# Kernel tuning notes

Hardware: AMD Instinct MI355X
Metric: run time of the kernel (lower is better)

The kernel has to match this reference:

```python
import jax, jax.numpy as jnp
import numpy as np

EMB = 64       # embedding_size
ATT = 32       # att_embedding_size (per-head dim)
HEADS = 4      # head_num
OUT = ATT * HEADS


def setup_inputs() -> dict:
    key = jax.random.key(0)
    ks = jax.random.split(key, 9)
    B, F = 16384, 40
    x = jax.random.normal(ks[0], (B, F, EMB), dtype=jnp.float32)
    # nn.Linear params: weight [out, in], bias [out]
    s = 0.05
    Wq = jax.random.normal(ks[1], (OUT, EMB), dtype=jnp.float32) * s
    bq = jax.random.normal(ks[2], (OUT,), dtype=jnp.float32) * s
    Wk = jax.random.normal(ks[3], (OUT, EMB), dtype=jnp.float32) * s
    bk = jax.random.normal(ks[4], (OUT,), dtype=jnp.float32) * s
    Wv = jax.random.normal(ks[5], (OUT, EMB), dtype=jnp.float32) * s
    bv = jax.random.normal(ks[6], (OUT,), dtype=jnp.float32) * s
    Wr = jax.random.normal(ks[7], (OUT, EMB), dtype=jnp.float32) * s
    br = jax.random.normal(ks[8], (OUT,), dtype=jnp.float32) * s
    return {"x": x, "Wq": Wq, "bq": bq, "Wk": Wk, "bk": bk,
            "Wv": Wv, "bv": bv, "Wr": Wr, "br": br}


def reference(x, Wq, bq, Wk, bk, Wv, bv, Wr, br):
    B, F, E = x.shape
    H, D = HEADS, ATT
    # QKV projections; split along last dim + cat along batch == reshape to heads
    q = (jnp.einsum('bfe,oe->bfo', x, Wq) + bq).reshape(B, F, H, D)
    k = (jnp.einsum('bfe,oe->bfo', x, Wk) + bk).reshape(B, F, H, D)
    v = (jnp.einsum('bfe,oe->bfo', x, Wv) + bv).reshape(B, F, H, D)
    # scaled dot-product attention over fields; NOTE: original scales by
    # sqrt(embedding_size), not sqrt(att_embedding_size)
    scale = 1.0 / jnp.sqrt(jnp.float32(E))
    att = jnp.einsum('bfhd,bghd->bhfg', q, k) * scale  # [B,H,F,F]
    att = jax.nn.softmax(att, axis=-1)                 # dropout_p = 0.0
    out = jnp.einsum('bhfg,bghd->bfhd', att, v).reshape(B, F, H * D)
    res = jnp.einsum('bfe,oe->bfo', x, Wr) + br        # use_res=True
    return jax.nn.relu(out + res)
```

## Files before the change

### kernel.cpp

```cpp
#include <hip/hip_runtime.h>
#include <hip/hip_bf16.h>


#define F_DIM 40
#define O_DIM 128

typedef __bf16 bf16x8 __attribute__((ext_vector_type(8)));
typedef __bf16 bf16x2 __attribute__((ext_vector_type(2)));
typedef float  f32x4  __attribute__((ext_vector_type(4)));

#define XBS 68
#define QS  40
#define VTS 72
#define OSS 44
#define HB0 3264
#define HSZ 5504
#define TOT 25280

static __device__ __forceinline__ unsigned pk2(float a, float b) {
  bf16x2 t;
  t[0] = (__bf16)a;
  t[1] = (__bf16)b;
  return __builtin_bit_cast(unsigned, t);
}
union V8 { uint2 u2[2]; uint4 u4; unsigned u[4]; bf16x8 v; };
static __device__ __forceinline__ bf16x8 lds_ld8(const unsigned short* p) {
  V8 t; t.u2[0] = *(const uint2*)p; t.u2[1] = *(const uint2*)(p + 4); return t.v;
}
static __device__ __forceinline__ bf16x8 lds_ld16(const unsigned short* p) {
  V8 t; t.u4 = *(const uint4*)p; return t.v;
}
static __device__ __forceinline__ f32x4 mfma16(bf16x8 a, bf16x8 b, f32x4 c) {
  return __builtin_amdgcn_mfma_f32_16x16x32_bf16(a, b, c, 0, 0, 0);
}

#if __has_builtin(__builtin_amdgcn_exp2f)
#define EXP2F __builtin_amdgcn_exp2f
#else
#define EXP2F exp2f
#endif
#if __has_builtin(__builtin_amdgcn_rcpf)
#define RCPF __builtin_amdgcn_rcpf
#else
#define RCPF(x) (1.0f / (x))
#endif

__global__ void convert_weights(const float* __restrict__ Wq, const float* __restrict__ Wk,
                                const float* __restrict__ Wv, const float* __restrict__ Wr,
                                unsigned short* __restrict__ ws) {
  int i = blockIdx.x * 256 + threadIdx.x;
  const float* src = (i < 8192) ? Wq : (i < 16384) ? Wk : (i < 24576) ? Wv : Wr;
  ws[i] = __builtin_bit_cast(unsigned short, (__bf16)src[i & 8191]);
}

__global__ __launch_bounds__(256, 3) void interact_kernel(
    const float* __restrict__ x, const unsigned short* __restrict__ wbf,
    const float* __restrict__ bq, const float* __restrict__ bk,
    const float* __restrict__ bv, const float* __restrict__ br,
    float* __restrict__ out) {
  __shared__ __align__(16) unsigned short sm[TOT];
  const int t = threadIdx.x;
  const int w = t >> 6;
  const int l = t & 63;
  const int c = l & 15;
  const int q = l >> 4;
  const int b = blockIdx.x;
  f32x4 z4 = {0.f, 0.f, 0.f, 0.f};

  const float* xp = x + (size_t)b * (F_DIM * 64);
  for (int i = t; i < 640; i += 256) {
    float4 v4 = reinterpret_cast<const float4*>(xp)[i];
    int f = i >> 4, e4 = (i & 15) << 2;
    uint2 pk; pk.x = pk2(v4.x, v4.y); pk.y = pk2(v4.z, v4.w);
    *reinterpret_cast<uint2*>(sm + f * XBS + e4) = pk;
  }
  {
    uint2 z; z.x = 0; z.y = 0;
    for (int i = t; i < 136; i += 256)
      reinterpret_cast<uint2*>(sm + 40 * XBS)[i] = z;
  }
  __syncthreads();

  const int hb = HB0 + w * HSZ;
  unsigned short* Qb  = sm + hb;
  unsigned short* Kb  = Qb + 1600;
  unsigned short* Vtb = Qb + 3200;

  bf16x8 xf[3][2];
#pragma unroll
  for (int nt = 0; nt < 3; ++nt)
#pragma unroll
    for (int ks = 0; ks < 2; ++ks)
      xf[nt][ks] = lds_ld8(sm + (c + 16 * nt) * XBS + 32 * ks + 8 * q);

  {
    const unsigned short* Wm[2] = { wbf + 32 * w * 64, wbf + 8192 + 32 * w * 64 };
    const float* Bp[2] = { bq, bk };
    unsigned short* Db[2] = { Qb, Kb };
#pragma unroll
    for (int pr = 0; pr < 2; ++pr) {
#pragma unroll
      for (int mt = 0; mt < 2; ++mt) {
        const unsigned short* wr0 = Wm[pr] + (16 * mt + c) * 64 + 8 * q;
        bf16x8 a0 = *reinterpret_cast<const bf16x8*>(wr0);
        bf16x8 a1 = *reinterpret_cast<const bf16x8*>(wr0 + 32);
        float4 bb = *reinterpret_cast<const float4*>(Bp[pr] + 32 * w + 16 * mt + 4 * q);
#pragma unroll
        for (int nt = 0; nt < 3; ++nt) {
          f32x4 acc = mfma16(a1, xf[nt][1], mfma16(a0, xf[nt][0], z4));
          int f = c + 16 * nt;
          if (f < 40) {
            uint2 pk;
            pk.x = pk2(acc[0] + bb.x, acc[1] + bb.y);
            pk.y = pk2(acc[2] + bb.z, acc[3] + bb.w);
            *reinterpret_cast<uint2*>(Db[pr] + f * QS + 16 * mt + 4 * q) = pk;
          }
        }
      }
    }
  }
#pragma unroll
  for (int nt = 0; nt < 2; ++nt) {
    const unsigned short* wr0 = wbf + 2 * 8192 + (32 * w + 16 * nt + c) * 64 + 8 * q;
    bf16x8 b0 = *reinterpret_cast<const bf16x8*>(wr0);
    bf16x8 b1 = *reinterpret_cast<const bf16x8*>(wr0 + 32);
    float bb = bv[32 * w + c + 16 * nt];
#pragma unroll
    for (int mt = 0; mt < 3; ++mt) {
      f32x4 acc = mfma16(xf[mt][1], b1, mfma16(xf[mt][0], b0, z4));
      uint2 pk;
      pk.x = pk2(acc[0] + bb, acc[1] + bb);
      pk.y = pk2(acc[2] + bb, acc[3] + bb);
      *reinterpret_cast<uint2*>(Vtb + (c + 16 * nt) * VTS + 16 * mt + 4 * q) = pk;
    }
  }
  {
    uint2 zz; zz.x = 0; zz.y = 0;
#pragma unroll
    for (int k2 = 0; k2 < 2; ++k2) {
      int idx = l + 64 * k2, row = idx >> 2, g4 = idx & 3;
      *reinterpret_cast<uint2*>(Vtb + row * VTS + 48 + 4 * g4) = zz;
    }
  }
  f32x4 rr[3][2];
#pragma unroll
  for (int nt = 0; nt < 2; ++nt) {
    const unsigned short* wr0 = wbf + 3 * 8192 + (32 * w + 16 * nt + c) * 64 + 8 * q;
    bf16x8 b0 = *reinterpret_cast<const bf16x8*>(wr0);
    bf16x8 b1 = *reinterpret_cast<const bf16x8*>(wr0 + 32);
#pragma unroll
    for (int mt = 0; mt < 3; ++mt)
      rr[mt][nt] = mfma16(xf[mt][1], b1, mfma16(xf[mt][0], b0, z4));
  }

  f32x4 s[3][3];
  {
    bf16x8 kf[3], qf[3];
#pragma unroll
    for (int gt = 0; gt < 3; ++gt) kf[gt] = lds_ld16(Kb + (c + 16 * gt) * QS + 8 * q);
#pragma unroll
    for (int ft = 0; ft < 3; ++ft) qf[ft] = lds_ld16(Qb + (c + 16 * ft) * QS + 8 * q);
#pragma unroll
    for (int gt = 0; gt < 3; ++gt)
#pragma unroll
      for (int ft = 0; ft < 3; ++ft)
        s[gt][ft] = mfma16(kf[gt], qf[ft], z4);
  }
  unsigned pp[3][3][2];
  const float cexp = 0.125f * 1.44269504f;
#pragma unroll
  for (int ft = 0; ft < 3; ++ft) {
    float m = -1e30f;
#pragma unroll
    for (int gt = 0; gt < 2; ++gt)
#pragma unroll
      for (int r = 0; r < 4; ++r) m = fmaxf(m, s[gt][ft][r]);
    if (q < 2) {
#pragma unroll
      for (int r = 0; r < 4; ++r) m = fmaxf(m, s[2][ft][r]);
    }
    m = fmaxf(m, __shfl_xor(m, 16, 64));
    m = fmaxf(m, __shfl_xor(m, 32, 64));
    float p[3][4]; float sum = 0.f;
#pragma unroll
    for (int gt = 0; gt < 3; ++gt)
#pragma unroll
      for (int r = 0; r < 4; ++r) {
        float pe = EXP2F((s[gt][ft][r] - m) * cexp);
        if (gt == 2 && q >= 2) pe = 0.f;
        p[gt][r] = pe; sum += pe;
      }
    sum += __shfl_xor(sum, 16, 64);
    sum += __shfl_xor(sum, 32, 64);
    float inv = RCPF(sum);
#pragma unroll
    for (int gt = 0; gt < 3; ++gt) {
      pp[ft][gt][0] = pk2(p[gt][0] * inv, p[gt][1] * inv);
      pp[ft][gt][1] = pk2(p[gt][2] * inv, p[gt][3] * inv);
    }
  }

  bf16x8 pf[3][2];
#pragma unroll
  for (int mt = 0; mt < 3; ++mt) {
    V8 f0, f1;
#pragma unroll
    for (int a = 0; a < 4; ++a) {
      int src = 16 * ((2 * q + (a >> 1)) & 3) + c;
      unsigned v0 = (unsigned)__shfl((int)pp[mt][0][a & 1], src, 64);
      unsigned v1 = (unsigned)__shfl((int)pp[mt][1][a & 1], src, 64);
      unsigned v2 = (unsigned)__shfl((int)pp[mt][2][a & 1], src, 64);
      f0.u[a] = (q < 2) ? v0 : v1;
      f1.u[a] = (q < 2) ? v2 : 0u;
    }
    pf[mt][0] = f0.v; pf[mt][1] = f1.v;
  }

  f32x4 o[3][2];
  {
    bf16x8 vb[2][2];
#pragma unroll
    for (int nt = 0; nt < 2; ++nt)
#pragma unroll
      for (int ks = 0; ks < 2; ++ks)
        vb[nt][ks] = lds_ld16(Vtb + (c + 16 * nt) * VTS + 32 * ks + 8 * q);
#pragma unroll
    for (int mt = 0; mt < 3; ++mt)
#pragma unroll
      for (int nt = 0; nt < 2; ++nt)
        o[mt][nt] = mfma16(pf[mt][1], vb[nt][1], mfma16(pf[mt][0], vb[nt][0], z4));
  }

  float* os = reinterpret_cast<float*>(sm + hb);
  float brv0 = br[32 * w + c], brv1 = br[32 * w + c + 16];
#pragma unroll
  for (int mt = 0; mt < 3; ++mt) {
    if (mt < 2 || q < 2) {
#pragma unroll
      for (int nt = 0; nt < 2; ++nt) {
        float bb = nt ? brv1 : brv0;
#pragma unroll
        for (int r = 0; r < 4; ++r) {
          int f = 16 * mt + 4 * q + r;
          os[f * OSS + c + 16 * nt] = fmaxf(o[mt][nt][r] + rr[mt][nt][r] + bb, 0.f);
        }
      }
    }
  }
  float* op = out + (size_t)b * (F_DIM * O_DIM) + 32 * w;
#pragma unroll
  for (int it = 0; it < 5; ++it) {
    int i = 64 * it + l;
    int f = i >> 3, d4 = i & 7;
    float4 v = *reinterpret_cast<const float4*>(os + f * OSS + 4 * d4);
    *reinterpret_cast<float4*>(op + (size_t)f * O_DIM + 4 * d4) = v;
  }
}

extern "C" void kernel_launch(void* const* d_in, const int* in_sizes, int n_in,
                              void* d_out, int out_size, void* d_ws, size_t ws_size,
                              hipStream_t stream) {
  const float* x  = (const float*)d_in[0];
  const float* Wq = (const float*)d_in[1];
  const float* bq = (const float*)d_in[2];
  const float* Wk = (const float*)d_in[3];
  const float* bk = (const float*)d_in[4];
  const float* Wv = (const float*)d_in[5];
  const float* bv = (const float*)d_in[6];
  const float* Wr = (const float*)d_in[7];
  const float* br = (const float*)d_in[8];
  unsigned short* wbf = (unsigned short*)d_ws;
  float* out = (float*)d_out;
  convert_weights<<<128, 256, 0, stream>>>(Wq, Wk, Wv, Wr, wbf);
  interact_kernel<<<16384, 256, 0, stream>>>(x, wbf, bq, bk, bv, br, out);
}
```

Measured before the change: 590.5 us.

## Keep Q/K in registers via shuffles, shrink LDS, raise occupancy target

Q and K projections are now turned into MFMA operand fragments with cross-lane shuffles instead of a round trip through shared memory. The per-wave LDS region shrinks to hold only V-transpose, and launch bounds rise from 3 to 6 blocks per CU. The residual projection is kept packed in bf16 to save registers, and output is written directly to global memory without LDS staging. The goal is less LDS traffic and higher occupancy, at the risk of uncoalesced scalar global stores, extra residual rounding to bf16, and register pressure under the tighter bound.

```diff
diff --git a/kernel.cpp b/kernel.cpp
--- a/kernel.cpp
+++ b/kernel.cpp
@@ -10,18 +10,20 @@
 typedef float  f32x4  __attribute__((ext_vector_type(4)));
 
 #define XBS 68
-#define QS  40
 #define VTS 72
-#define OSS 44
 #define HB0 3264
-#define HSZ 5504
-#define TOT 25280
+#define HSZ 2304
+#define TOT 12480
 
 static __device__ __forceinline__ unsigned pk2(float a, float b) {
   bf16x2 t;
   t[0] = (__bf16)a;
   t[1] = (__bf16)b;
   return __builtin_bit_cast(unsigned, t);
+}
+static __device__ __forceinline__ float bf2f(unsigned short h) {
+  unsigned u = ((unsigned)h) << 16;
+  return __builtin_bit_cast(float, u);
 }
 union V8 { uint2 u2[2]; uint4 u4; unsigned u[4]; bf16x8 v; };
 static __device__ __forceinline__ bf16x8 lds_ld8(const unsigned short* p) {
@@ -53,7 +55,7 @@
   ws[i] = __builtin_bit_cast(unsigned short, (__bf16)src[i & 8191]);
 }
 
-__global__ __launch_bounds__(256, 3) void interact_kernel(
+__global__ __launch_bounds__(256, 6) void interact_kernel(
     const float* __restrict__ x, const unsigned short* __restrict__ wbf,
     const float* __restrict__ bq, const float* __restrict__ bk,
     const float* __restrict__ bv, const float* __restrict__ br,
@@ -67,6 +69,9 @@
   const int b = blockIdx.x;
   f32x4 z4 = {0.f, 0.f, 0.f, 0.f};
 
+  const int srcA0 = 16 * (2 * (q & 1) + 0) + c;
+  const int srcA1 = 16 * (2 * (q & 1) + 1) + c;
+
   const float* xp = x + (size_t)b * (F_DIM * 64);
   for (int i = t; i < 640; i += 256) {
     float4 v4 = reinterpret_cast<const float4*>(xp)[i];
@@ -81,10 +86,7 @@
   }
   __syncthreads();
 
-  const int hb = HB0 + w * HSZ;
-  unsigned short* Qb  = sm + hb;
-  unsigned short* Kb  = Qb + 1600;
-  unsigned short* Vtb = Qb + 3200;
+  unsigned short* Vtb = sm + HB0 + w * HSZ;
 
   bf16x8 xf[3][2];
 #pragma unroll
@@ -93,32 +95,6 @@
     for (int ks = 0; ks < 2; ++ks)
       xf[nt][ks] = lds_ld8(sm + (c + 16 * nt) * XBS + 32 * ks + 8 * q);
 
-  {
-    const unsigned short* Wm[2] = { wbf + 32 * w * 64, wbf + 8192 + 32 * w * 64 };
-    const float* Bp[2] = { bq, bk };
-    unsigned short* Db[2] = { Qb, Kb };
-#pragma unroll
-    for (int pr = 0; pr < 2; ++pr) {
-#pragma unroll
-      for (int mt = 0; mt < 2; ++mt) {
-        const unsigned short* wr0 = Wm[pr] + (16 * mt + c) * 64 + 8 * q;
-        bf16x8 a0 = *reinterpret_cast<const bf16x8*>(wr0);
-        bf16x8 a1 = *reinterpret_cast<const bf16x8*>(wr0 + 32);
-        float4 bb = *reinterpret_cast<const float4*>(Bp[pr] + 32 * w + 16 * mt + 4 * q);
-#pragma unroll
-        for (int nt = 0; nt < 3; ++nt) {
-          f32x4 acc = mfma16(a1, xf[nt][1], mfma16(a0, xf[nt][0], z4));
-          int f = c + 16 * nt;
-          if (f < 40) {
-            uint2 pk;
-            pk.x = pk2(acc[0] + bb.x, acc[1] + bb.y);
-            pk.y = pk2(acc[2] + bb.z, acc[3] + bb.w);
-            *reinterpret_cast<uint2*>(Db[pr] + f * QS + 16 * mt + 4 * q) = pk;
-          }
-        }
-      }
-    }
-  }
 #pragma unroll
   for (int nt = 0; nt < 2; ++nt) {
     const unsigned short* wr0 = wbf + 2 * 8192 + (32 * w + 16 * nt + c) * 64 + 8 * q;
@@ -142,31 +118,60 @@
       *reinterpret_cast<uint2*>(Vtb + row * VTS + 48 + 4 * g4) = zz;
     }
   }
-  f32x4 rr[3][2];
+  unsigned rp[3][2][2];
 #pragma unroll
   for (int nt = 0; nt < 2; ++nt) {
     const unsigned short* wr0 = wbf + 3 * 8192 + (32 * w + 16 * nt + c) * 64 + 8 * q;
     bf16x8 b0 = *reinterpret_cast<const bf16x8*>(wr0);
     bf16x8 b1 = *reinterpret_cast<const bf16x8*>(wr0 + 32);
 #pragma unroll
-    for (int mt = 0; mt < 3; ++mt)
-      rr[mt][nt] = mfma16(xf[mt][1], b1, mfma16(xf[mt][0], b0, z4));
+    for (int mt = 0; mt < 3; ++mt) {
+      f32x4 acc = mfma16(xf[mt][1], b1, mfma16(xf[mt][0], b0, z4));
+      rp[mt][nt][0] = pk2(acc[0], acc[1]);
+      rp[mt][nt][1] = pk2(acc[2], acc[3]);
+    }
+  }
+  bf16x8 qf[3], kf[3];
+#pragma unroll
+  for (int pr = 0; pr < 2; ++pr) {
+    const unsigned short* Wm = wbf + pr * 8192 + 32 * w * 64;
+    const float* Bp = pr ? bk : bq;
+    unsigned qk[3][2][2];
+#pragma unroll
+    for (int mt = 0; mt < 2; ++mt) {
+      const unsigned short* wr0 = Wm + (16 * mt + c) * 64 + 8 * q;
+      bf16x8 a0 = *reinterpret_cast<const bf16x8*>(wr0);
+      bf16x8 a1 = *reinterpret_cast<const bf16x8*>(wr0 + 32);
+      float4 bb = *reinterpret_cast<const float4*>(Bp + 32 * w + 16 * mt + 4 * q);
+#pragma unroll
+      for (int nt = 0; nt < 3; ++nt) {
+        f32x4 acc = mfma16(a1, xf[nt][1], mfma16(a0, xf[nt][0], z4));
+        qk[nt][mt][0] = pk2(acc[0] + bb.x, acc[1] + bb.y);
+        qk[nt][mt][1] = pk2(acc[2] + bb.z, acc[3] + bb.w);
+      }
+    }
+#pragma unroll
+    for (int gt = 0; gt < 3; ++gt) {
+      V8 f;
+#pragma unroll
+      for (int a = 0; a < 4; ++a) {
+        int src = (a < 2) ? srcA0 : srcA1;
+        unsigned v0 = (unsigned)__shfl((int)qk[gt][0][a & 1], src, 64);
+        unsigned v1 = (unsigned)__shfl((int)qk[gt][1][a & 1], src, 64);
+        f.u[a] = (q < 2) ? v0 : v1;
+      }
+      if (pr) kf[gt] = f.v; else qf[gt] = f.v;
+    }
   }
 
   f32x4 s[3][3];
-  {
-    bf16x8 kf[3], qf[3];
-#pragma unroll
-    for (int gt = 0; gt < 3; ++gt) kf[gt] = lds_ld16(Kb + (c + 16 * gt) * QS + 8 * q);
-#pragma unroll
-    for (int ft = 0; ft < 3; ++ft) qf[ft] = lds_ld16(Qb + (c + 16 * ft) * QS + 8 * q);
-#pragma unroll
-    for (int gt = 0; gt < 3; ++gt)
-#pragma unroll
-      for (int ft = 0; ft < 3; ++ft)
-        s[gt][ft] = mfma16(kf[gt], qf[ft], z4);
-  }
-  unsigned pp[3][3][2];
+#pragma unroll
+  for (int gt = 0; gt < 3; ++gt)
+#pragma unroll
+    for (int ft = 0; ft < 3; ++ft)
+      s[gt][ft] = mfma16(kf[gt], qf[ft], z4);
+
+  bf16x8 pf[3][2];
   const float cexp = 0.125f * 1.44269504f;
 #pragma unroll
   for (int ft = 0; ft < 3; ++ft) {
@@ -193,27 +198,23 @@
     sum += __shfl_xor(sum, 16, 64);
     sum += __shfl_xor(sum, 32, 64);
     float inv = RCPF(sum);
+    unsigned pp[3][2];
 #pragma unroll
     for (int gt = 0; gt < 3; ++gt) {
-      pp[ft][gt][0] = pk2(p[gt][0] * inv, p[gt][1] * inv);
-      pp[ft][gt][1] = pk2(p[gt][2] * inv, p[gt][3] * inv);
-    }
-  }
-
-  bf16x8 pf[3][2];
-#pragma unroll
-  for (int mt = 0; mt < 3; ++mt) {
+      pp[gt][0] = pk2(p[gt][0] * inv, p[gt][1] * inv);
+      pp[gt][1] = pk2(p[gt][2] * inv, p[gt][3] * inv);
+    }
     V8 f0, f1;
 #pragma unroll
     for (int a = 0; a < 4; ++a) {
-      int src = 16 * ((2 * q + (a >> 1)) & 3) + c;
-      unsigned v0 = (unsigned)__shfl((int)pp[mt][0][a & 1], src, 64);
-      unsigned v1 = (unsigned)__shfl((int)pp[mt][1][a & 1], src, 64);
-      unsigned v2 = (unsigned)__shfl((int)pp[mt][2][a & 1], src, 64);
+      int src = (a < 2) ? srcA0 : srcA1;
+      unsigned v0 = (unsigned)__shfl((int)pp[0][a & 1], src, 64);
+      unsigned v1 = (unsigned)__shfl((int)pp[1][a & 1], src, 64);
+      unsigned v2 = (unsigned)__shfl((int)pp[2][a & 1], src, 64);
       f0.u[a] = (q < 2) ? v0 : v1;
       f1.u[a] = (q < 2) ? v2 : 0u;
     }
-    pf[mt][0] = f0.v; pf[mt][1] = f1.v;
+    pf[ft][0] = f0.v; pf[ft][1] = f1.v;
   }
 
   f32x4 o[3][2];
@@ -231,8 +232,8 @@
         o[mt][nt] = mfma16(pf[mt][1], vb[nt][1], mfma16(pf[mt][0], vb[nt][0], z4));
   }
 
-  float* os = reinterpret_cast<float*>(sm + hb);
   float brv0 = br[32 * w + c], brv1 = br[32 * w + c + 16];
+  float* op = out + (size_t)b * (F_DIM * O_DIM) + 32 * w;
 #pragma unroll
   for (int mt = 0; mt < 3; ++mt) {
     if (mt < 2 || q < 2) {
@@ -242,18 +243,12 @@
 #pragma unroll
         for (int r = 0; r < 4; ++r) {
           int f = 16 * mt + 4 * q + r;
-          os[f * OSS + c + 16 * nt] = fmaxf(o[mt][nt][r] + rr[mt][nt][r] + bb, 0.f);
+          unsigned pr_ = rp[mt][nt][r >> 1];
+          float rv = bf2f((unsigned short)((r & 1) ? (pr_ >> 16) : (pr_ & 0xFFFFu)));
+          op[(size_t)f * O_DIM + c + 16 * nt] = fmaxf(o[mt][nt][r] + rv + bb, 0.f);
         }
       }
     }
-  }
-  float* op = out + (size_t)b * (F_DIM * O_DIM) + 32 * w;
-#pragma unroll
-  for (int it = 0; it < 5; ++it) {
-    int i = 64 * it + l;
-    int f = i >> 3, d4 = i & 7;
-    float4 v = *reinterpret_cast<const float4*>(os + f * OSS + 4 * d4);
-    *reinterpret_cast<float4*>(op + (size_t)f * O_DIM + 4 * d4) = v;
   }
 }
 
```

After: 627.1 us. 1.06x slower.
